# Performance work log

Measured on AMD Instinct MI355X. Metric: run time of the kernel, lower is better.

Reference implementation:

```python
import jax, jax.numpy as jnp
import numpy as np

B, NC, NP, K, C, DIN, TS, M = 4, 1024, 32768, 3, 256, 448, 2, 4
EPS = 1e-5


def _mlp3(x, w0, b0, w1, b1, w2, b2):
    x = jax.nn.relu(x @ w0 + b0)
    x = jax.nn.relu(x @ w1 + b1)
    return x @ w2 + b2


def setup_inputs():
    key = jax.random.key(0)
    ks = jax.random.split(key, 32)
    f = lambda i, shape, s=0.02: jax.random.normal(ks[i], shape, jnp.float32) * s
    iw = jax.random.uniform(ks[0], (B, NP, K), jnp.float32)
    iw = iw / iw.sum(-1, keepdims=True)  # KNN interpolation weights sum to 1
    return {
        'pc_embeddings': f(1, (B, NC, DIN), 1.0),
        'pc_pe': f(2, (B, NC, C), 1.0),
        'sparse_prompt': f(3, (B, TS, C), 1.0),
        'dense_prompt': f(4, (B, NC, C), 1.0),
        'pf_feat': f(5, (B, NP, DIN), 1.0),
        'interp_weight': iw,
        'interp_index': jax.random.randint(ks[6], (B, NP, K), 0, NC),
        'iou_token': f(7, (1, C)),
        'mask_tokens': f(8, (M, C)),
        'enc_w0': f(9, (DIN, C)), 'enc_b0': jnp.zeros((C,), jnp.float32),
        'enc_w1': f(10, (C, C)), 'enc_b1': jnp.zeros((C,), jnp.float32),
        'enc_w2': f(11, (C, C)), 'enc_b2': jnp.zeros((C,), jnp.float32),
        'up_w0': f(12, (C + DIN, C)), 'up_b0': jnp.zeros((C,), jnp.float32),
        'ln_g': jnp.ones((C,), jnp.float32), 'ln_b': jnp.zeros((C,), jnp.float32),
        'up_w1': f(13, (C, C)), 'up_b1': jnp.zeros((C,), jnp.float32),
        'hyp_w0': f(14, (M, C, C)), 'hyp_b0': jnp.zeros((M, C), jnp.float32),
        'hyp_w1': f(15, (M, C, C)), 'hyp_b1': jnp.zeros((M, C), jnp.float32),
        'hyp_w2': f(16, (M, C, C)), 'hyp_b2': jnp.zeros((M, C), jnp.float32),
        'iou_w0': f(17, (C, 256)), 'iou_b0': jnp.zeros((256,), jnp.float32),
        'iou_w1': f(18, (256, 256)), 'iou_b1': jnp.zeros((256,), jnp.float32),
        'iou_w2': f(19, (256, M)), 'iou_b2': jnp.zeros((M,), jnp.float32),
    }


def reference(pc_embeddings, pc_pe, sparse_prompt, dense_prompt, pf_feat,
              interp_weight, interp_index, iou_token, mask_tokens,
              enc_w0, enc_b0, enc_w1, enc_b1, enc_w2, enc_b2,
              up_w0, up_b0, ln_g, ln_b, up_w1, up_b1,
              hyp_w0, hyp_b0, hyp_w1, hyp_b1, hyp_w2, hyp_b2,
              iou_w0, iou_b0, iou_w1, iou_b1, iou_w2, iou_b2):
    # encoder_mapper: MLP 448 -> 256 (relu between layers)
    pc_emb = _mlp3(pc_embeddings, enc_w0, enc_b0, enc_w1, enc_b1, enc_w2, enc_b2)
    out_tok = jnp.concatenate([iou_token, mask_tokens], 0)  # [1+M, C]
    tokens = jnp.concatenate(
        [jnp.broadcast_to(out_tok[None], (B, 1 + M, C)), sparse_prompt], 1)
    src = pc_emb + dense_prompt  # [B, NC, C]
    # transformer stand-in (identity): hs = tokens, src unchanged; pc_pe unused
    hs = tokens
    iou_token_out = hs[:, 0]            # [B, C]
    mask_tokens_out = hs[:, 1:1 + M]    # [B, M, C]
    # interpolate_features: irregular gather of k=3 neighbor center embeddings
    idx = interp_index.astype(jnp.int32).reshape(B, NP * K, 1)
    gathered = jnp.take_along_axis(src, idx, axis=1).reshape(B, NP, K, C)
    interp = (gathered * interp_weight[..., None]).sum(2)  # [B, NP, C]
    x = jnp.concatenate([interp, pf_feat], -1)  # [B, NP, C+448]
    # output_upscaling: Linear -> LayerNorm -> GELU -> Linear -> GELU
    x = x @ up_w0 + up_b0
    mu = x.mean(-1, keepdims=True)
    var = ((x - mu) ** 2).mean(-1, keepdims=True)
    x = (x - mu) * jax.lax.rsqrt(var + EPS) * ln_g + ln_b
    x = jax.nn.gelu(x, approximate=False)
    upscaled = jax.nn.gelu(x @ up_w1 + up_b1, approximate=False)  # [B, NP, C]
    # per-mask-token hypernetwork MLPs (batched over the M tokens)
    h = jax.nn.relu(jnp.einsum('bmc,mcd->bmd', mask_tokens_out, hyp_w0) + hyp_b0[None])
    h = jax.nn.relu(jnp.einsum('bmc,mcd->bmd', h, hyp_w1) + hyp_b1[None])
    hyper = jnp.einsum('bmc,mcd->bmd', h, hyp_w2) + hyp_b2[None]
    hyper = hyper[:, 1:]  # multimask_output=True -> slice(1, None)
    masks = jnp.einsum('bmc,bnc->bmn', hyper, upscaled)  # [B, M-1, NP]
    iou_pred = _mlp3(iou_token_out, iou_w0, iou_b0, iou_w1, iou_b1, iou_w2, iou_b2)[:, 1:]
    return masks, iou_pred
```

## Files before the change

### kernel.cpp

```cpp
#include <hip/hip_runtime.h>
#include <hip/hip_bf16.h>
#include <math.h>

constexpr int kB   = 4;
constexpr int kNC  = 1024;
constexpr int kNP  = 32768;
constexpr int kC   = 256;
constexpr int kDIN = 448;
constexpr int kM   = 4;

typedef __attribute__((ext_vector_type(8))) short short8;
typedef __attribute__((ext_vector_type(4))) float float4v;

__device__ __forceinline__ float gelu_exact(float x) {
    return 0.5f * x * (1.0f + erff(x * 0.70710678118654752440f));
}
__device__ __forceinline__ unsigned short f2bf(float f) {
    unsigned int u = __float_as_uint(f);
    unsigned int r = (u + 0x7fffu + ((u >> 16) & 1u)) >> 16;
    return (unsigned short)r;
}
__device__ __forceinline__ float bf2f(unsigned short s) {
    return __uint_as_float(((unsigned int)s) << 16);
}
__device__ __forceinline__ unsigned int pk_bf16(float lo, float hi) {
    __hip_bfloat162 h = __float22bfloat162_rn(float2{lo, hi});
    union { __hip_bfloat162 h; unsigned int u; } c;
    c.h = h;
    return c.u;
}

__global__ __launch_bounds__(256) void prep_weights(
    const float* __restrict__ ew0, const float* __restrict__ ew1,
    const float* __restrict__ ew2, const float* __restrict__ uw0,
    const float* __restrict__ uw1,
    unsigned short* __restrict__ ew0s, unsigned short* __restrict__ ew1s,
    unsigned short* __restrict__ ew2s, unsigned short* __restrict__ w0as,
    unsigned short* __restrict__ w0bs, unsigned short* __restrict__ w1s_)
{
    const int bx = blockIdx.x, t = threadIdx.x;
    const float* srcW; int k0; unsigned short* dst;
    if (bx < 14)      { srcW = ew0; k0 = bx * 32;              dst = ew0s + bx * 8192; }
    else if (bx < 22) { srcW = ew1; k0 = (bx - 14) * 32;       dst = ew1s + (bx - 14) * 8192; }
    else if (bx < 30) { srcW = ew2; k0 = (bx - 22) * 32;       dst = ew2s + (bx - 22) * 8192; }
    else if (bx < 38) { srcW = uw0; k0 = (bx - 30) * 32;       dst = w0as + (bx - 30) * 8192; }
    else if (bx < 52) { srcW = uw0; k0 = 256 + (bx - 38) * 32; dst = w0bs + (bx - 38) * 8192; }
    else              { srcW = uw1; k0 = (bx - 52) * 32;       dst = w1s_ + (bx - 52) * 8192; }
    unsigned short v[32];
    #pragma unroll
    for (int kk = 0; kk < 32; ++kk) v[kk] = f2bf(srcW[(size_t)(k0 + kk) * kC + t]);
    #pragma unroll
    for (int j = 0; j < 4; ++j) *(short8*)(dst + t * 32 + j * 8) = *(short8*)(v + j * 8);
}

__device__ __forceinline__ void gemm_x2_global(
    const unsigned short* __restrict__ x2e, const unsigned short* __restrict__ wsrc,
    int nchunk, int w, int q, int ml, float4v acc[4][4])
{
    const unsigned short* wp[4];
    #pragma unroll
    for (int ct = 0; ct < 4; ++ct) wp[ct] = wsrc + ((64 * w + 16 * ct + ml) * 32 + q * 8);
    for (int c = 0; c < nchunk; ++c) {
        short8 af[4], bfr[4];
        #pragma unroll
        for (int rt = 0; rt < 4; ++rt)
            af[rt] = *(const short8*)(x2e + (16 * rt + ml) * 264 + c * 32 + q * 8);
        #pragma unroll
        for (int ct = 0; ct < 4; ++ct) bfr[ct] = *(const short8*)(wp[ct] + c * 8192);
        #pragma unroll
        for (int rt = 0; rt < 4; ++rt)
            #pragma unroll
            for (int ct = 0; ct < 4; ++ct)
                acc[rt][ct] = __builtin_amdgcn_mfma_f32_16x16x32_bf16(af[rt], bfr[ct], acc[rt][ct], 0, 0, 0);
    }
}

__global__ __launch_bounds__(256) void kernelA(
    const float* __restrict__ pc, const float* __restrict__ dense,
    const unsigned short* __restrict__ ew0s, const float* __restrict__ eb0,
    const unsigned short* __restrict__ ew1s, const float* __restrict__ eb1,
    const unsigned short* __restrict__ ew2s, const float* __restrict__ eb2,
    const unsigned short* __restrict__ w0as, const float* __restrict__ ub0,
    const float* __restrict__ iou_token, const float* __restrict__ mask_tokens,
    const float* __restrict__ hw0, const float* __restrict__ hb0,
    const float* __restrict__ hw1, const float* __restrict__ hb1,
    const float* __restrict__ hw2, const float* __restrict__ hb2,
    const float* __restrict__ iw0, const float* __restrict__ ib0,
    const float* __restrict__ iw1, const float* __restrict__ ib1,
    const float* __restrict__ iw2, const float* __restrict__ ib2,
    unsigned short* __restrict__ Zbf,
    float* __restrict__ hyper_out,
    float* __restrict__ iou_out)
{
    __shared__ unsigned short x2e[64 * 264];
    __shared__ float va[kC];
    __shared__ float vb[kC];
    const int tid = threadIdx.x, bx = blockIdx.x;

    if (bx < 64) {
        const int row0 = bx * 64;
        const int w = tid >> 6, lane = tid & 63, q = lane >> 4, ml = lane & 15;

        const float* pcr[4];
        #pragma unroll
        for (int rt = 0; rt < 4; ++rt) pcr[rt] = pc + (size_t)(row0 + 16 * rt + ml) * kDIN;
        float4v acc[4][4] = {};
        for (int c = 0; c < 14; ++c) {
            short8 af[4], bfr[4];
            #pragma unroll
            for (int rt = 0; rt < 4; ++rt) {
                float4 f0 = *(const float4*)(pcr[rt] + c * 32 + q * 8);
                float4 f1 = *(const float4*)(pcr[rt] + c * 32 + q * 8 + 4);
                union { short8 s; unsigned int u[4]; } cv;
                cv.u[0] = pk_bf16(f0.x, f0.y); cv.u[1] = pk_bf16(f0.z, f0.w);
                cv.u[2] = pk_bf16(f1.x, f1.y); cv.u[3] = pk_bf16(f1.z, f1.w);
                af[rt] = cv.s;
            }
            #pragma unroll
            for (int ct = 0; ct < 4; ++ct)
                bfr[ct] = *(const short8*)(ew0s + (size_t)c * 8192 + (64 * w + 16 * ct + ml) * 32 + q * 8);
            #pragma unroll
            for (int rt = 0; rt < 4; ++rt)
                #pragma unroll
                for (int ct = 0; ct < 4; ++ct)
                    acc[rt][ct] = __builtin_amdgcn_mfma_f32_16x16x32_bf16(af[rt], bfr[ct], acc[rt][ct], 0, 0, 0);
        }
        {
            float bc[4];
            #pragma unroll
            for (int ct = 0; ct < 4; ++ct) bc[ct] = eb0[64 * w + 16 * ct + ml];
            #pragma unroll
            for (int rt = 0; rt < 4; ++rt)
                #pragma unroll
                for (int i = 0; i < 4; ++i) {
                    int row = 16 * rt + 4 * q + i;
                    #pragma unroll
                    for (int ct = 0; ct < 4; ++ct)
                        x2e[row * 264 + 64 * w + 16 * ct + ml] = f2bf(fmaxf(acc[rt][ct][i] + bc[ct], 0.0f));
                }
        }
        __syncthreads();

        float4v acc2[4][4] = {};
        gemm_x2_global(x2e, ew1s, 8, w, q, ml, acc2);
        __syncthreads();
        {
            float bc[4];
            #pragma unroll
            for (int ct = 0; ct < 4; ++ct) bc[ct] = eb1[64 * w + 16 * ct + ml];
            #pragma unroll
            for (int rt = 0; rt < 4; ++rt)
                #pragma unroll
                for (int i = 0; i < 4; ++i) {
                    int row = 16 * rt + 4 * q + i;
                    #pragma unroll
                    for (int ct = 0; ct < 4; ++ct)
                        x2e[row * 264 + 64 * w + 16 * ct + ml] = f2bf(fmaxf(acc2[rt][ct][i] + bc[ct], 0.0f));
                }
        }
        __syncthreads();

        float4v acc3[4][4] = {};
        gemm_x2_global(x2e, ew2s, 8, w, q, ml, acc3);
        __syncthreads();
        {
            float bc[4];
            #pragma unroll
            for (int ct = 0; ct < 4; ++ct) bc[ct] = eb2[64 * w + 16 * ct + ml];
            #pragma unroll
            for (int rt = 0; rt < 4; ++rt)
                #pragma unroll
                for (int i = 0; i < 4; ++i) {
                    int row = 16 * rt + 4 * q + i;
                    #pragma unroll
                    for (int ct = 0; ct < 4; ++ct) {
                        int col = 64 * w + 16 * ct + ml;
                        float v = acc3[rt][ct][i] + bc[ct] + dense[(size_t)(row0 + row) * kC + col];
                        x2e[row * 264 + col] = f2bf(v);
                    }
                }
        }
        __syncthreads();

        float4v accZ[4][4] = {};
        gemm_x2_global(x2e, w0as, 8, w, q, ml, accZ);
        {
            float bc[4];
            #pragma unroll
            for (int ct = 0; ct < 4; ++ct) bc[ct] = ub0[64 * w + 16 * ct + ml];
            #pragma unroll
            for (int rt = 0; rt < 4; ++rt)
                #pragma unroll
                for (int i = 0; i < 4; ++i) {
                    int row = 16 * rt + 4 * q + i;
                    #pragma unroll
                    for (int ct = 0; ct < 4; ++ct) {
                        int col = 64 * w + 16 * ct + ml;
                        Zbf[(size_t)(row0 + row) * kC + col] = f2bf(accZ[rt][ct][i] + bc[ct]);
                    }
                }
        }
    } else if (bx < 68) {
        const int m = bx - 64;
        va[tid] = mask_tokens[m * kC + tid];
        __syncthreads();
        const float* W = hw0 + (size_t)m * kC * kC;
        float acc = hb0[m * kC + tid];
        for (int d = 0; d < kC; d++) acc = fmaf(va[d], W[d * kC + tid], acc);
        vb[tid] = fmaxf(acc, 0.0f);
        __syncthreads();
        W = hw1 + (size_t)m * kC * kC;
        acc = hb1[m * kC + tid];
        for (int d = 0; d < kC; d++) acc = fmaf(vb[d], W[d * kC + tid], acc);
        va[tid] = fmaxf(acc, 0.0f);
        __syncthreads();
        W = hw2 + (size_t)m * kC * kC;
        acc = hb2[m * kC + tid];
        for (int d = 0; d < kC; d++) acc = fmaf(va[d], W[d * kC + tid], acc);
        if (m >= 1) hyper_out[(m - 1) * kC + tid] = acc;
    } else {
        va[tid] = iou_token[tid];
        __syncthreads();
        float acc = ib0[tid];
        for (int d = 0; d < kC; d++) acc = fmaf(va[d], iw0[d * 256 + tid], acc);
        vb[tid] = fmaxf(acc, 0.0f);
        __syncthreads();
        acc = ib1[tid];
        for (int d = 0; d < 256; d++) acc = fmaf(vb[d], iw1[d * 256 + tid], acc);
        va[tid] = fmaxf(acc, 0.0f);
        __syncthreads();
        if (tid < kM) {
            acc = ib2[tid];
            for (int d = 0; d < 256; d++) acc = fmaf(va[d], iw2[d * kM + tid], acc);
            if (tid >= 1)
                for (int b = 0; b < kB; b++) iou_out[b * 3 + (tid - 1)] = acc;
        }
    }
}

__global__ __launch_bounds__(256, 3) void main_mfma(
    const unsigned short* __restrict__ Zbf,
    const float* __restrict__ pf,
    const float* __restrict__ iwgt, const int* __restrict__ iidx,
    const unsigned short* __restrict__ w0bs, const unsigned short* __restrict__ w1s_,
    const float* __restrict__ lng, const float* __restrict__ lnb,
    const float* __restrict__ b1v, const float* __restrict__ hyper,
    float* __restrict__ masks)
{
    __shared__ unsigned short x2[64 * 264];
    __shared__ int   gi[64][3];
    __shared__ float gw[64][3];
    __shared__ float sums[4][64];
    __shared__ float sqs[4][64];
    __shared__ float muA[64];
    __shared__ float rsA[64];
    __shared__ float pd[12][64];

    const int b = blockIdx.y, p0 = blockIdx.x * 64, tid = threadIdx.x;
    const int w = tid >> 6, lane = tid & 63, q = lane >> 4, ml = lane & 15;

    if (tid < 192) {
        int r = tid / 3, k = tid - r * 3;
        int base = (b * kNP + p0 + r) * 3 + k;
        gi[r][k] = iidx[base];
        gw[r][k] = iwgt[base];
    }
    __syncthreads();

    const float* pfr[4];
    #pragma unroll
    for (int rt = 0; rt < 4; ++rt)
        pfr[rt] = pf + ((size_t)b * kNP + p0 + 16 * rt + ml) * kDIN;
    const unsigned short* wbp[4];
    #pragma unroll
    for (int ct = 0; ct < 4; ++ct) wbp[ct] = w0bs + ((64 * w + 16 * ct + ml) * 32 + q * 8);

    float4v acc[4][4] = {};
    for (int c = 0; c < 14; ++c) {
        short8 af[4], bfr[4];
        #pragma unroll
        for (int rt = 0; rt < 4; ++rt) {
            float4 f0 = *(const float4*)(pfr[rt] + c * 32 + q * 8);
            float4 f1 = *(const float4*)(pfr[rt] + c * 32 + q * 8 + 4);
            union { short8 s; unsigned int u[4]; } cv;
            cv.u[0] = pk_bf16(f0.x, f0.y); cv.u[1] = pk_bf16(f0.z, f0.w);
            cv.u[2] = pk_bf16(f1.x, f1.y); cv.u[3] = pk_bf16(f1.z, f1.w);
            af[rt] = cv.s;
        }
        #pragma unroll
        for (int ct = 0; ct < 4; ++ct) bfr[ct] = *(const short8*)(wbp[ct] + c * 8192);
        #pragma unroll
        for (int rt = 0; rt < 4; ++rt)
            #pragma unroll
            for (int ct = 0; ct < 4; ++ct)
                acc[rt][ct] = __builtin_amdgcn_mfma_f32_16x16x32_bf16(af[rt], bfr[ct], acc[rt][ct], 0, 0, 0);
    }

    {
        const unsigned short* zb = Zbf + (size_t)b * kNC * kC;
        #pragma unroll
        for (int rt = 0; rt < 4; ++rt)
            #pragma unroll
            for (int i = 0; i < 4; ++i) {
                int row = 16 * rt + 4 * q + i;
                #pragma unroll
                for (int k = 0; k < 3; ++k) {
                    float wk = gw[row][k];
                    const unsigned short* zr = zb + (size_t)gi[row][k] * kC + 64 * w + ml;
                    #pragma unroll
                    for (int ct = 0; ct < 4; ++ct)
                        acc[rt][ct][i] = fmaf(wk, bf2f(zr[16 * ct]), acc[rt][ct][i]);
                }
            }
    }

    {
        float s[4][4], s2[4][4];
        #pragma unroll
        for (int rt = 0; rt < 4; ++rt)
            #pragma unroll
            for (int i = 0; i < 4; ++i) {
                float a = 0.f, b2 = 0.f;
                #pragma unroll
                for (int ct = 0; ct < 4; ++ct) {
                    float v = acc[rt][ct][i];
                    a += v; b2 = fmaf(v, v, b2);
                }
                s[rt][i] = a; s2[rt][i] = b2;
            }
        #pragma unroll
        for (int o = 1; o < 16; o <<= 1) {
            #pragma unroll
            for (int rt = 0; rt < 4; ++rt)
                #pragma unroll
                for (int i = 0; i < 4; ++i) {
                    s[rt][i]  += __shfl_xor(s[rt][i], o);
                    s2[rt][i] += __shfl_xor(s2[rt][i], o);
                }
        }
        if (ml == 0) {
            #pragma unroll
            for (int rt = 0; rt < 4; ++rt)
                #pragma unroll
                for (int i = 0; i < 4; ++i) {
                    int row = 16 * rt + 4 * q + i;
                    sums[w][row] = s[rt][i];
                    sqs[w][row]  = s2[rt][i];
                }
        }
    }
    __syncthreads();
    if (tid < 64) {
        float ts = sums[0][tid] + sums[1][tid] + sums[2][tid] + sums[3][tid];
        float tq = sqs[0][tid] + sqs[1][tid] + sqs[2][tid] + sqs[3][tid];
        float mu = ts * (1.0f / 256.0f);
        float var = tq * (1.0f / 256.0f) - mu * mu;
        muA[tid] = mu;
        rsA[tid] = rsqrtf(var + 1e-5f);
    }
    __syncthreads();

    {
        float gc[4], oc[4];
        #pragma unroll
        for (int ct = 0; ct < 4; ++ct) {
            gc[ct] = lng[64 * w + 16 * ct + ml];
            oc[ct] = lnb[64 * w + 16 * ct + ml];
        }
        #pragma unroll
        for (int rt = 0; rt < 4; ++rt)
            #pragma unroll
            for (int i = 0; i < 4; ++i) {
                int row = 16 * rt + 4 * q + i;
                float mu = muA[row], rs = rsA[row];
                #pragma unroll
                for (int ct = 0; ct < 4; ++ct) {
                    float v = (acc[rt][ct][i] - mu) * rs * gc[ct] + oc[ct];
                    x2[row * 264 + 64 * w + 16 * ct + ml] = f2bf(gelu_exact(v));
                }
            }
    }
    __syncthreads();

    float4v acc2[4][4] = {};
    gemm_x2_global(x2, w1s_, 8, w, q, ml, acc2);

    {
        float bc1[4], hy[3][4];
        #pragma unroll
        for (int ct = 0; ct < 4; ++ct) bc1[ct] = b1v[64 * w + 16 * ct + ml];
        #pragma unroll
        for (int m = 0; m < 3; ++m)
            #pragma unroll
            for (int ct = 0; ct < 4; ++ct) hy[m][ct] = hyper[m * kC + 64 * w + 16 * ct + ml];
        float pdl[3][4][4] = {};
        #pragma unroll
        for (int rt = 0; rt < 4; ++rt)
            #pragma unroll
            for (int ct = 0; ct < 4; ++ct)
                #pragma unroll
                for (int i = 0; i < 4; ++i) {
                    float u = gelu_exact(acc2[rt][ct][i] + bc1[ct]);
                    #pragma unroll
                    for (int m = 0; m < 3; ++m) pdl[m][rt][i] = fmaf(u, hy[m][ct], pdl[m][rt][i]);
                }
        #pragma unroll
        for (int o = 1; o < 16; o <<= 1) {
            #pragma unroll
            for (int m = 0; m < 3; ++m)
                #pragma unroll
                for (int rt = 0; rt < 4; ++rt)
                    #pragma unroll
                    for (int i = 0; i < 4; ++i)
                        pdl[m][rt][i] += __shfl_xor(pdl[m][rt][i], o);
        }
        if (ml < 3) {
            const int m = ml;
            #pragma unroll
            for (int rt = 0; rt < 4; ++rt)
                #pragma unroll
                for (int i = 0; i < 4; ++i)
                    pd[w * 3 + m][16 * rt + 4 * q + i] = pdl[m][rt][i];
        }
    }
    __syncthreads();
    if (tid < 192) {
        int m = tid >> 6, r = tid & 63;
        float v = pd[0 + m][r] + pd[3 + m][r] + pd[6 + m][r] + pd[9 + m][r];
        masks[((size_t)b * 3 + m) * kNP + p0 + r] = v;
    }
}

extern "C" void kernel_launch(void* const* d_in, const int* in_sizes, int n_in,
                              void* d_out, int out_size, void* d_ws, size_t ws_size,
                              hipStream_t stream) {
    const float* pc_emb  = (const float*)d_in[0];
    const float* dense   = (const float*)d_in[3];
    const float* pf      = (const float*)d_in[4];
    const float* iwgt    = (const float*)d_in[5];
    const int*   iidx    = (const int*)d_in[6];
    const float* iou_tok = (const float*)d_in[7];
    const float* mtok    = (const float*)d_in[8];
    const float* ew0 = (const float*)d_in[9];
    const float* eb0 = (const float*)d_in[10];
    const float* ew1 = (const float*)d_in[11];
    const float* eb1 = (const float*)d_in[12];
    const float* ew2 = (const float*)d_in[13];
    const float* eb2 = (const float*)d_in[14];
    const float* uw0 = (const float*)d_in[15];
    const float* ub0 = (const float*)d_in[16];
    const float* lng = (const float*)d_in[17];
    const float* lnb = (const float*)d_in[18];
    const float* uw1 = (const float*)d_in[19];
    const float* ub1 = (const float*)d_in[20];
    const float* hw0 = (const float*)d_in[21];
    const float* hb0 = (const float*)d_in[22];
    const float* hw1 = (const float*)d_in[23];
    const float* hb1 = (const float*)d_in[24];
    const float* hw2 = (const float*)d_in[25];
    const float* hb2 = (const float*)d_in[26];
    const float* iw0 = (const float*)d_in[27];
    const float* ib0 = (const float*)d_in[28];
    const float* iw1 = (const float*)d_in[29];
    const float* ib1 = (const float*)d_in[30];
    const float* iw2 = (const float*)d_in[31];
    const float* ib2 = (const float*)d_in[32];

    float* out = (float*)d_out;

    char* ws = (char*)d_ws;
    unsigned short* Zbf  = (unsigned short*)(ws + 0);
    float* ws_hyper      = (float*)(ws + 2097152);
    unsigned short* ew0s = (unsigned short*)(ws + 2100224);
    unsigned short* ew1s = (unsigned short*)(ws + 2329600);
    unsigned short* ew2s = (unsigned short*)(ws + 2460672);
    unsigned short* w0as = (unsigned short*)(ws + 2591744);
    unsigned short* w0bs = (unsigned short*)(ws + 2722816);
    unsigned short* w1s_ = (unsigned short*)(ws + 2952192);

    prep_weights<<<60, 256, 0, stream>>>(ew0, ew1, ew2, uw0, uw1,
                                         ew0s, ew1s, ew2s, w0as, w0bs, w1s_);

    kernelA<<<69, 256, 0, stream>>>(
        pc_emb, dense, ew0s, eb0, ew1s, eb1, ew2s, eb2, w0as, ub0,
        iou_tok, mtok, hw0, hb0, hw1, hb1, hw2, hb2,
        iw0, ib0, iw1, ib1, iw2, ib2,
        Zbf, ws_hyper, out + (size_t)kB * 3 * kNP);

    main_mfma<<<dim3(kNP / 64, kB), 256, 0, stream>>>(
        Zbf, pf, iwgt, iidx, w0bs, w1s_,
        lng, lnb, ub1, ws_hyper, out);
}
```

Before: 638.9 us.

## Split encoder kernel into 16-row blocks and vectorize Z gather with permuted layout

kernelA's encoder path now processes 16 rows per block instead of 64, raising the grid from 69 to 261 blocks so the small encoder GEMM chain fills more compute units. The hypernetwork and IoU blocks move to the front indices. Z is stored with a permuted column layout so each lane writes, and the main kernel gathers, four bf16 values with one 8-byte access instead of four strided scalar loads. The smaller tiles re-read the weights more often per row.

```diff
diff --git a/kernel.cpp b/kernel.cpp
--- a/kernel.cpp
+++ b/kernel.cpp
@@ -11,6 +11,7 @@
 
 typedef __attribute__((ext_vector_type(8))) short short8;
 typedef __attribute__((ext_vector_type(4))) float float4v;
+typedef __attribute__((ext_vector_type(4))) unsigned short ushort4v;
 
 __device__ __forceinline__ float gelu_exact(float x) {
     return 0.5f * x * (1.0f + erff(x * 0.70710678118654752440f));
@@ -75,6 +76,24 @@
     }
 }
 
+__device__ __forceinline__ void gemm_x1_global(
+    const unsigned short* __restrict__ x2e, const unsigned short* __restrict__ wsrc,
+    int nchunk, int w, int q, int ml, float4v acc[4])
+{
+    const unsigned short* wp[4];
+    #pragma unroll
+    for (int ct = 0; ct < 4; ++ct) wp[ct] = wsrc + ((64 * w + 16 * ct + ml) * 32 + q * 8);
+    for (int c = 0; c < nchunk; ++c) {
+        short8 af = *(const short8*)(x2e + ml * 264 + c * 32 + q * 8);
+        short8 bfr[4];
+        #pragma unroll
+        for (int ct = 0; ct < 4; ++ct) bfr[ct] = *(const short8*)(wp[ct] + c * 8192);
+        #pragma unroll
+        for (int ct = 0; ct < 4; ++ct)
+            acc[ct] = __builtin_amdgcn_mfma_f32_16x16x32_bf16(af, bfr[ct], acc[ct], 0, 0, 0);
+    }
+}
+
 __global__ __launch_bounds__(256) void kernelA(
     const float* __restrict__ pc, const float* __restrict__ dense,
     const unsigned short* __restrict__ ew0s, const float* __restrict__ eb0,
@@ -92,116 +111,98 @@
     float* __restrict__ hyper_out,
     float* __restrict__ iou_out)
 {
-    __shared__ unsigned short x2e[64 * 264];
+    __shared__ unsigned short x2e[16 * 264];
     __shared__ float va[kC];
     __shared__ float vb[kC];
     const int tid = threadIdx.x, bx = blockIdx.x;
 
-    if (bx < 64) {
-        const int row0 = bx * 64;
+    if (bx >= 5) {
+        const int row0 = (bx - 5) * 16;
         const int w = tid >> 6, lane = tid & 63, q = lane >> 4, ml = lane & 15;
 
-        const float* pcr[4];
-        #pragma unroll
-        for (int rt = 0; rt < 4; ++rt) pcr[rt] = pc + (size_t)(row0 + 16 * rt + ml) * kDIN;
-        float4v acc[4][4] = {};
+        const float* pcr = pc + (size_t)(row0 + ml) * kDIN;
+        float4v acc0[4] = {};
         for (int c = 0; c < 14; ++c) {
-            short8 af[4], bfr[4];
-            #pragma unroll
-            for (int rt = 0; rt < 4; ++rt) {
-                float4 f0 = *(const float4*)(pcr[rt] + c * 32 + q * 8);
-                float4 f1 = *(const float4*)(pcr[rt] + c * 32 + q * 8 + 4);
-                union { short8 s; unsigned int u[4]; } cv;
-                cv.u[0] = pk_bf16(f0.x, f0.y); cv.u[1] = pk_bf16(f0.z, f0.w);
-                cv.u[2] = pk_bf16(f1.x, f1.y); cv.u[3] = pk_bf16(f1.z, f1.w);
-                af[rt] = cv.s;
-            }
-            #pragma unroll
-            for (int ct = 0; ct < 4; ++ct)
-                bfr[ct] = *(const short8*)(ew0s + (size_t)c * 8192 + (64 * w + 16 * ct + ml) * 32 + q * 8);
-            #pragma unroll
-            for (int rt = 0; rt < 4; ++rt)
-                #pragma unroll
-                for (int ct = 0; ct < 4; ++ct)
-                    acc[rt][ct] = __builtin_amdgcn_mfma_f32_16x16x32_bf16(af[rt], bfr[ct], acc[rt][ct], 0, 0, 0);
+            float4 f0 = *(const float4*)(pcr + c * 32 + q * 8);
+            float4 f1 = *(const float4*)(pcr + c * 32 + q * 8 + 4);
+            union { short8 s; unsigned int u[4]; } cv;
+            cv.u[0] = pk_bf16(f0.x, f0.y); cv.u[1] = pk_bf16(f0.z, f0.w);
+            cv.u[2] = pk_bf16(f1.x, f1.y); cv.u[3] = pk_bf16(f1.z, f1.w);
+            short8 af = cv.s;
+            #pragma unroll
+            for (int ct = 0; ct < 4; ++ct) {
+                short8 bfr = *(const short8*)(ew0s + (size_t)c * 8192 + (64 * w + 16 * ct + ml) * 32 + q * 8);
+                acc0[ct] = __builtin_amdgcn_mfma_f32_16x16x32_bf16(af, bfr, acc0[ct], 0, 0, 0);
+            }
         }
         {
             float bc[4];
             #pragma unroll
             for (int ct = 0; ct < 4; ++ct) bc[ct] = eb0[64 * w + 16 * ct + ml];
             #pragma unroll
-            for (int rt = 0; rt < 4; ++rt)
-                #pragma unroll
-                for (int i = 0; i < 4; ++i) {
-                    int row = 16 * rt + 4 * q + i;
-                    #pragma unroll
-                    for (int ct = 0; ct < 4; ++ct)
-                        x2e[row * 264 + 64 * w + 16 * ct + ml] = f2bf(fmaxf(acc[rt][ct][i] + bc[ct], 0.0f));
-                }
-        }
-        __syncthreads();
-
-        float4v acc2[4][4] = {};
-        gemm_x2_global(x2e, ew1s, 8, w, q, ml, acc2);
+            for (int i = 0; i < 4; ++i) {
+                int row = 4 * q + i;
+                #pragma unroll
+                for (int ct = 0; ct < 4; ++ct)
+                    x2e[row * 264 + 64 * w + 16 * ct + ml] = f2bf(fmaxf(acc0[ct][i] + bc[ct], 0.0f));
+            }
+        }
+        __syncthreads();
+
+        float4v acc2[4] = {};
+        gemm_x1_global(x2e, ew1s, 8, w, q, ml, acc2);
         __syncthreads();
         {
             float bc[4];
             #pragma unroll
             for (int ct = 0; ct < 4; ++ct) bc[ct] = eb1[64 * w + 16 * ct + ml];
             #pragma unroll
-            for (int rt = 0; rt < 4; ++rt)
-                #pragma unroll
-                for (int i = 0; i < 4; ++i) {
-                    int row = 16 * rt + 4 * q + i;
-                    #pragma unroll
-                    for (int ct = 0; ct < 4; ++ct)
-                        x2e[row * 264 + 64 * w + 16 * ct + ml] = f2bf(fmaxf(acc2[rt][ct][i] + bc[ct], 0.0f));
-                }
-        }
-        __syncthreads();
-
-        float4v acc3[4][4] = {};
-        gemm_x2_global(x2e, ew2s, 8, w, q, ml, acc3);
+            for (int i = 0; i < 4; ++i) {
+                int row = 4 * q + i;
+                #pragma unroll
+                for (int ct = 0; ct < 4; ++ct)
+                    x2e[row * 264 + 64 * w + 16 * ct + ml] = f2bf(fmaxf(acc2[ct][i] + bc[ct], 0.0f));
+            }
+        }
+        __syncthreads();
+
+        float4v acc3[4] = {};
+        gemm_x1_global(x2e, ew2s, 8, w, q, ml, acc3);
         __syncthreads();
         {
             float bc[4];
             #pragma unroll
             for (int ct = 0; ct < 4; ++ct) bc[ct] = eb2[64 * w + 16 * ct + ml];
             #pragma unroll
-            for (int rt = 0; rt < 4; ++rt)
-                #pragma unroll
-                for (int i = 0; i < 4; ++i) {
-                    int row = 16 * rt + 4 * q + i;
-                    #pragma unroll
-                    for (int ct = 0; ct < 4; ++ct) {
-                        int col = 64 * w + 16 * ct + ml;
-                        float v = acc3[rt][ct][i] + bc[ct] + dense[(size_t)(row0 + row) * kC + col];
-                        x2e[row * 264 + col] = f2bf(v);
-                    }
-                }
-        }
-        __syncthreads();
-
-        float4v accZ[4][4] = {};
-        gemm_x2_global(x2e, w0as, 8, w, q, ml, accZ);
+            for (int i = 0; i < 4; ++i) {
+                int row = 4 * q + i;
+                #pragma unroll
+                for (int ct = 0; ct < 4; ++ct) {
+                    int col = 64 * w + 16 * ct + ml;
+                    float v = acc3[ct][i] + bc[ct] + dense[(size_t)(row0 + row) * kC + col];
+                    x2e[row * 264 + col] = f2bf(v);
+                }
+            }
+        }
+        __syncthreads();
+
+        float4v accZ[4] = {};
+        gemm_x1_global(x2e, w0as, 8, w, q, ml, accZ);
         {
             float bc[4];
             #pragma unroll
             for (int ct = 0; ct < 4; ++ct) bc[ct] = ub0[64 * w + 16 * ct + ml];
             #pragma unroll
-            for (int rt = 0; rt < 4; ++rt)
-                #pragma unroll
-                for (int i = 0; i < 4; ++i) {
-                    int row = 16 * rt + 4 * q + i;
-                    #pragma unroll
-                    for (int ct = 0; ct < 4; ++ct) {
-                        int col = 64 * w + 16 * ct + ml;
-                        Zbf[(size_t)(row0 + row) * kC + col] = f2bf(accZ[rt][ct][i] + bc[ct]);
-                    }
-                }
-        }
-    } else if (bx < 68) {
-        const int m = bx - 64;
+            for (int i = 0; i < 4; ++i) {
+                int row = 4 * q + i;
+                ushort4v o;
+                #pragma unroll
+                for (int ct = 0; ct < 4; ++ct) o[ct] = f2bf(accZ[ct][i] + bc[ct]);
+                *(ushort4v*)(Zbf + (size_t)(row0 + row) * kC + 64 * w + 4 * ml) = o;
+            }
+        }
+    } else if (bx < 4) {
+        const int m = bx;
         va[tid] = mask_tokens[m * kC + tid];
         __syncthreads();
         const float* W = hw0 + (size_t)m * kC * kC;
@@ -297,7 +298,7 @@
     }
 
     {
-        const unsigned short* zb = Zbf + (size_t)b * kNC * kC;
+        const unsigned short* zb = Zbf + (size_t)b * kNC * kC + 64 * w + 4 * ml;
         #pragma unroll
         for (int rt = 0; rt < 4; ++rt)
             #pragma unroll
@@ -306,10 +307,10 @@
                 #pragma unroll
                 for (int k = 0; k < 3; ++k) {
                     float wk = gw[row][k];
-                    const unsigned short* zr = zb + (size_t)gi[row][k] * kC + 64 * w + ml;
+                    ushort4v z = *(const ushort4v*)(zb + (size_t)gi[row][k] * kC);
                     #pragma unroll
                     for (int ct = 0; ct < 4; ++ct)
-                        acc[rt][ct][i] = fmaf(wk, bf2f(zr[16 * ct]), acc[rt][ct][i]);
+                        acc[rt][ct][i] = fmaf(wk, bf2f(z[ct]), acc[rt][ct][i]);
                 }
             }
     }
@@ -481,7 +482,7 @@
     prep_weights<<<60, 256, 0, stream>>>(ew0, ew1, ew2, uw0, uw1,
                                          ew0s, ew1s, ew2s, w0as, w0bs, w1s_);
 
-    kernelA<<<69, 256, 0, stream>>>(
+    kernelA<<<261, 256, 0, stream>>>(
         pc_emb, dense, ew0s, eb0, ew1s, eb1, ew2s, eb2, w0as, ub0,
         iou_tok, mtok, hw0, hb0, hw1, hb1, hw2, hb2,
         iw0, ib0, iw1, ib1, iw2, ib2,
```

Measured after the change: 637.9 us. Within noise of the previous version (-0.2%).
